# Kernel optimization log

Hardware: AMD Instinct MI355X
Metric: run time of the kernel (lower is better)

## Reference

```python
import jax, jax.numpy as jnp
import numpy as np

EDGE_DIM = 3
NUM_HEADS = 8
HIDDEN = NUM_HEADS * 2  # 16
N = 2048
E = 65536


def setup_inputs() -> dict:
    key = jax.random.key(0)
    k1, k2, k3, k4, k5 = jax.random.split(key, 5)
    # xavier_uniform bounds: sqrt(6/(fan_in+fan_out))
    lim1 = float(np.sqrt(6.0 / (EDGE_DIM + HIDDEN)))
    lim2 = float(np.sqrt(6.0 / (HIDDEN + NUM_HEADS)))
    return {
        "edge_index": jax.random.randint(k1, (2, E), 0, N, dtype=jnp.int64)
        if jax.config.jax_enable_x64 else jax.random.randint(k1, (2, E), 0, N, dtype=jnp.int32),
        "edge_attr": jax.random.normal(k2, (E, EDGE_DIM), dtype=jnp.float32),
        "num_nodes": N,
        "W1": jax.random.uniform(k3, (EDGE_DIM, HIDDEN), jnp.float32, -lim1, lim1),
        "b1": jnp.zeros((HIDDEN,), jnp.float32),
        "W2": jax.random.uniform(k4, (HIDDEN, NUM_HEADS), jnp.float32, -lim2, lim2),
        "b2": jnp.zeros((NUM_HEADS,), jnp.float32),
    }


def reference(edge_index, edge_attr, num_nodes, W1, b1, W2, b2):
    # tiny MLP: (E,3) -> (E,16) -> relu -> (E,8)
    h = jax.nn.relu(edge_attr @ W1 + b1)
    edge_bias = h @ W2 + b2  # (E, H)
    src, dst = edge_index[0], edge_index[1]
    bias = jnp.zeros((num_nodes, num_nodes, NUM_HEADS), dtype=edge_bias.dtype)
    bias = bias.at[src, dst].set(edge_bias)
    return bias
```

## Files before the change

### kernel.cpp

```cpp
#include <hip/hip_runtime.h>
#include <math.h>

#define EDGE_DIM 3
#define NUM_HEADS 8
#define HIDDEN 16

typedef float float4v __attribute__((ext_vector_type(4)));

__device__ __forceinline__ void edge_mlp(const float a0, const float a1, const float a2,
                                         const float* __restrict__ W1,
                                         const float* __restrict__ b1,
                                         const float* __restrict__ W2,
                                         const float* __restrict__ b2,
                                         float* o ) {
    float h[HIDDEN];
#pragma unroll
    for (int j = 0; j < HIDDEN; ++j) {
        float s = b1[j];
        s += a0 * W1[0 * HIDDEN + j];
        s += a1 * W1[1 * HIDDEN + j];
        s += a2 * W1[2 * HIDDEN + j];
        h[j] = s > 0.0f ? s : 0.0f;
    }
#pragma unroll
    for (int i = 0; i < NUM_HEADS; ++i) {
        float s = b2[i];
#pragma unroll
        for (int j = 0; j < HIDDEN; ++j) s += h[j] * W2[j * NUM_HEADS + i];
        o[i] = s;
    }
}

__global__ void k_mark(const int* __restrict__ ei, float* __restrict__ out,
                       int E, int N) {
    int e = blockIdx.x * blockDim.x + threadIdx.x;
    if (e >= E) return;
    int src = ei[e];
    int dst = ei[E + e];
    size_t slot = (size_t)src * (size_t)N + (size_t)dst;
    unsigned* p = (unsigned*)(out + slot * NUM_HEADS);
    atomicMax(p, (unsigned)(e + 1));
}

__global__ void k_write(const int* __restrict__ ei, const float* __restrict__ ea,
                        const float* __restrict__ W1, const float* __restrict__ b1,
                        const float* __restrict__ W2, const float* __restrict__ b2,
                        float* __restrict__ out, int E, int N) {
    int e = blockIdx.x * blockDim.x + threadIdx.x;
    if (e >= E) return;
    int src = ei[e];
    int dst = ei[E + e];
    size_t slot = (size_t)src * (size_t)N + (size_t)dst;
    float* p = out + slot * NUM_HEADS;
    unsigned m = *(const unsigned*)p;
    if (m != (unsigned)(e + 1)) return;
    float o[NUM_HEADS];
    edge_mlp(ea[e * EDGE_DIM + 0], ea[e * EDGE_DIM + 1], ea[e * EDGE_DIM + 2],
             W1, b1, W2, b2, o);
    unsigned u = __float_as_uint(o[0]);
    if (u >= 1u && u <= (unsigned)E) o[0] = 0.0f;
    float4v lo = {o[0], o[1], o[2], o[3]};
    float4v hi = {o[4], o[5], o[6], o[7]};
    *(float4v*)p = lo;
    *(float4v*)(p + 4) = hi;
}

extern "C" void kernel_launch(void* const* d_in, const int* in_sizes, int n_in,
                              void* d_out, int out_size, void* d_ws, size_t ws_size,
                              hipStream_t stream) {
    const int* ei   = (const int*)d_in[0];
    const float* ea = (const float*)d_in[1];
    const float* W1 = (const float*)d_in[3];
    const float* b1 = (const float*)d_in[4];
    const float* W2 = (const float*)d_in[5];
    const float* b2 = (const float*)d_in[6];
    float* out = (float*)d_out;

    const int E = in_sizes[0] / 2;
    const int N = (int)(sqrt((double)(out_size / NUM_HEADS)) + 0.5);

    hipMemsetAsync(d_out, 0, (size_t)out_size * sizeof(float), stream);

    const int blk = 256;
    const int grid = (E + blk - 1) / blk;
    k_mark<<<grid, blk, 0, stream>>>(ei, out, E, N);
    k_write<<<grid, blk, 0, stream>>>(ei, ea, W1, b1, W2, b2, out, E, N);
}
```

Baseline: 33.06 us.

## Use compact workspace marker and fused fill kernel instead of output memset

When workspace is large enough, atomic last-writer markers go into a compact N*N uint array and per-edge MLP results into a workspace buffer. A single fill kernel then writes the whole output once, either zeros or the gathered edge bias, which replaces the full-output memset followed by scattered writes. The memset shrinks eightfold, but the fill kernel still writes the full 134MB output and adds a marker read plus indirect gathers. If the workspace is too small, the old path is kept as a fallback.

```diff
diff --git a/kernel.cpp b/kernel.cpp
--- a/kernel.cpp
+++ b/kernel.cpp
@@ -31,26 +31,58 @@
     }
 }
 
-__global__ void k_mark(const int* __restrict__ ei, float* __restrict__ out,
-                       int E, int N) {
+__global__ void k_mark_mlp(const int* __restrict__ ei, const float* __restrict__ ea,
+                           const float* __restrict__ W1, const float* __restrict__ b1,
+                           const float* __restrict__ W2, const float* __restrict__ b2,
+                           unsigned* __restrict__ marker, float4v* __restrict__ ebias,
+                           int E, int N) {
     int e = blockIdx.x * blockDim.x + threadIdx.x;
     if (e >= E) return;
+    float o[NUM_HEADS];
+    edge_mlp(ea[e * EDGE_DIM + 0], ea[e * EDGE_DIM + 1], ea[e * EDGE_DIM + 2],
+             W1, b1, W2, b2, o);
+    float4v lo = {o[0], o[1], o[2], o[3]};
+    float4v hi = {o[4], o[5], o[6], o[7]};
+    ebias[(size_t)e * 2 + 0] = lo;
+    ebias[(size_t)e * 2 + 1] = hi;
     int src = ei[e];
     int dst = ei[E + e];
     size_t slot = (size_t)src * (size_t)N + (size_t)dst;
-    unsigned* p = (unsigned*)(out + slot * NUM_HEADS);
-    atomicMax(p, (unsigned)(e + 1));
+    atomicMax(&marker[slot], (unsigned)(e + 1));
 }
 
-__global__ void k_write(const int* __restrict__ ei, const float* __restrict__ ea,
-                        const float* __restrict__ W1, const float* __restrict__ b1,
-                        const float* __restrict__ W2, const float* __restrict__ b2,
-                        float* __restrict__ out, int E, int N) {
+__global__ void k_fill(const unsigned* __restrict__ marker,
+                       const float4v* __restrict__ ebias,
+                       float4v* __restrict__ out, size_t nslots) {
+    size_t s = (size_t)blockIdx.x * blockDim.x + threadIdx.x;
+    if (s >= nslots) return;
+    unsigned m = marker[s];
+    float4v lo = {0.0f, 0.0f, 0.0f, 0.0f};
+    float4v hi = {0.0f, 0.0f, 0.0f, 0.0f};
+    if (m) {
+        size_t e = (size_t)(m - 1);
+        lo = ebias[e * 2 + 0];
+        hi = ebias[e * 2 + 1];
+    }
+    out[s * 2 + 0] = lo;
+    out[s * 2 + 1] = hi;
+}
+
+__global__ void k_mark_out(const int* __restrict__ ei, float* __restrict__ out,
+                           int E, int N) {
     int e = blockIdx.x * blockDim.x + threadIdx.x;
     if (e >= E) return;
-    int src = ei[e];
-    int dst = ei[E + e];
-    size_t slot = (size_t)src * (size_t)N + (size_t)dst;
+    size_t slot = (size_t)ei[e] * (size_t)N + (size_t)ei[E + e];
+    atomicMax((unsigned*)(out + slot * NUM_HEADS), (unsigned)(e + 1));
+}
+
+__global__ void k_write_out(const int* __restrict__ ei, const float* __restrict__ ea,
+                            const float* __restrict__ W1, const float* __restrict__ b1,
+                            const float* __restrict__ W2, const float* __restrict__ b2,
+                            float* __restrict__ out, int E, int N) {
+    int e = blockIdx.x * blockDim.x + threadIdx.x;
+    if (e >= E) return;
+    size_t slot = (size_t)ei[e] * (size_t)N + (size_t)ei[E + e];
     float* p = out + slot * NUM_HEADS;
     unsigned m = *(const unsigned*)p;
     if (m != (unsigned)(e + 1)) return;
@@ -78,11 +110,25 @@
 
     const int E = in_sizes[0] / 2;
     const int N = (int)(sqrt((double)(out_size / NUM_HEADS)) + 0.5);
+    const size_t nslots = (size_t)N * (size_t)N;
 
-    hipMemsetAsync(d_out, 0, (size_t)out_size * sizeof(float), stream);
+    const size_t marker_bytes = nslots * sizeof(unsigned);
+    const size_t ebias_bytes  = (size_t)E * NUM_HEADS * sizeof(float);
+    const int blk = 256;
+    const int egrid = (E + blk - 1) / blk;
 
-    const int blk = 256;
-    const int grid = (E + blk - 1) / blk;
-    k_mark<<<grid, blk, 0, stream>>>(ei, out, E, N);
-    k_write<<<grid, blk, 0, stream>>>(ei, ea, W1, b1, W2, b2, out, E, N);
+    if (ws_size >= marker_bytes + ebias_bytes) {
+        unsigned* marker = (unsigned*)d_ws;
+        float4v* ebias = (float4v*)((char*)d_ws + marker_bytes);
+
+        hipMemsetAsync(marker, 0, marker_bytes, stream);
+        k_mark_mlp<<<egrid, blk, 0, stream>>>(ei, ea, W1, b1, W2, b2,
+                                              marker, ebias, E, N);
+        const size_t sgrid = (nslots + blk - 1) / blk;
+        k_fill<<<(int)sgrid, blk, 0, stream>>>(marker, ebias, (float4v*)out, nslots);
+    } else {
+        hipMemsetAsync(d_out, 0, (size_t)out_size * sizeof(float), stream);
+        k_mark_out<<<egrid, blk, 0, stream>>>(ei, out, E, N);
+        k_write_out<<<egrid, blk, 0, stream>>>(ei, ea, W1, b1, W2, b2, out, E, N);
+    }
 }
```

After: 43.63 us. 1.32x slower.

## Replace output memset with bitmap-guided fill kernel that writes every slot

Applied to the files above, without the earlier changes.

Drops the full-output memset. The mark pass now resolves last-writer tags with a CAS loop and records touched slots in a workspace bitmap. A new fill kernel then writes every 16-byte output unit, emitting either zeros or the MLP result of the winning edge. The aim is to merge the clear and the scatter into one streaming write pass. The cost is extra bitmap traffic and reliance on workspace and output contents that are never cleared between calls: bmA only accumulates bits, and bmB is only ever cleared. This risks wrong results if stale tags or stale bits from earlier runs collide with the current edges.

```diff
diff --git a/kernel.cpp b/kernel.cpp
--- a/kernel.cpp
+++ b/kernel.cpp
@@ -32,25 +32,73 @@
 }
 
 __global__ void k_mark(const int* __restrict__ ei, float* __restrict__ out,
+                       unsigned long long* __restrict__ bmA,
+                       unsigned long long* __restrict__ bmB,
                        int E, int N) {
     int e = blockIdx.x * blockDim.x + threadIdx.x;
     if (e >= E) return;
-    int src = ei[e];
-    int dst = ei[E + e];
-    size_t slot = (size_t)src * (size_t)N + (size_t)dst;
+    size_t slot = (size_t)ei[e] * (size_t)N + (size_t)ei[E + e];
     unsigned* p = (unsigned*)(out + slot * NUM_HEADS);
-    atomicMax(p, (unsigned)(e + 1));
+    const unsigned my = (unsigned)(e + 1);
+
+    unsigned w = atomicOr(p, 0u);
+    while (true) {
+        bool is_tag = (w >= 1u && w <= (unsigned)E);
+        if (is_tag && w >= my) break;
+        unsigned old = atomicCAS(p, w, my);
+        if (old == w) break;
+        w = old;
+    }
+    atomicOr(&bmA[slot >> 6], 1ull << (slot & 63));
+    atomicAnd(&bmB[slot >> 6], ~(1ull << (slot & 63)));
 }
 
-__global__ void k_write(const int* __restrict__ ei, const float* __restrict__ ea,
-                        const float* __restrict__ W1, const float* __restrict__ b1,
-                        const float* __restrict__ W2, const float* __restrict__ b2,
-                        float* __restrict__ out, int E, int N) {
+__global__ __launch_bounds__(256) void k_fill(
+        const unsigned long long* __restrict__ bmA,
+        const unsigned long long* __restrict__ bmB,
+        const int* __restrict__ ei, const float* __restrict__ ea,
+        const float* __restrict__ W1, const float* __restrict__ b1,
+        const float* __restrict__ W2, const float* __restrict__ b2,
+        float4v* __restrict__ out4, int E, int N, size_t nunits) {
+    size_t u = (size_t)blockIdx.x * 256 + threadIdx.x;
+    if (u >= nunits) return;
+    size_t s = u >> 1;
+    float4v v = {0.0f, 0.0f, 0.0f, 0.0f};
+    unsigned long long bm = bmA[s >> 6] & ~bmB[s >> 6];
+    if ((bm >> (s & 63)) & 1ull) {
+        unsigned t = ((const unsigned*)&out4[s << 1])[0];
+        if (t >= 1u && t <= (unsigned)E) {
+            unsigned e = t - 1u;
+            size_t es = (size_t)ei[e] * (size_t)N + (size_t)ei[(size_t)E + e];
+            if (es == s) {
+                float o[NUM_HEADS];
+                edge_mlp(ea[(size_t)e * EDGE_DIM + 0], ea[(size_t)e * EDGE_DIM + 1],
+                         ea[(size_t)e * EDGE_DIM + 2], W1, b1, W2, b2, o);
+                unsigned u0 = __float_as_uint(o[0]);
+                if (u0 >= 1u && u0 <= (unsigned)E) o[0] = 0.0f;
+                if (u & 1) { v[0] = o[4]; v[1] = o[5]; v[2] = o[6]; v[3] = o[7]; }
+                else       { v[0] = o[0]; v[1] = o[1]; v[2] = o[2]; v[3] = o[3]; }
+            }
+        }
+    }
+    out4[u] = v;
+}
+
+__global__ void k_mark_out(const int* __restrict__ ei, float* __restrict__ out,
+                           int E, int N) {
     int e = blockIdx.x * blockDim.x + threadIdx.x;
     if (e >= E) return;
-    int src = ei[e];
-    int dst = ei[E + e];
-    size_t slot = (size_t)src * (size_t)N + (size_t)dst;
+    size_t slot = (size_t)ei[e] * (size_t)N + (size_t)ei[E + e];
+    atomicMax((unsigned*)(out + slot * NUM_HEADS), (unsigned)(e + 1));
+}
+
+__global__ void k_write_out(const int* __restrict__ ei, const float* __restrict__ ea,
+                            const float* __restrict__ W1, const float* __restrict__ b1,
+                            const float* __restrict__ W2, const float* __restrict__ b2,
+                            float* __restrict__ out, int E, int N) {
+    int e = blockIdx.x * blockDim.x + threadIdx.x;
+    if (e >= E) return;
+    size_t slot = (size_t)ei[e] * (size_t)N + (size_t)ei[E + e];
     float* p = out + slot * NUM_HEADS;
     unsigned m = *(const unsigned*)p;
     if (m != (unsigned)(e + 1)) return;
@@ -78,11 +126,23 @@
 
     const int E = in_sizes[0] / 2;
     const int N = (int)(sqrt((double)(out_size / NUM_HEADS)) + 0.5);
-
-    hipMemsetAsync(d_out, 0, (size_t)out_size * sizeof(float), stream);
+    const size_t nslots = (size_t)N * (size_t)N;
+    const size_t nunits = nslots * 2;
+    const size_t nwords = (nslots + 63) / 64;
 
     const int blk = 256;
-    const int grid = (E + blk - 1) / blk;
-    k_mark<<<grid, blk, 0, stream>>>(ei, out, E, N);
-    k_write<<<grid, blk, 0, stream>>>(ei, ea, W1, b1, W2, b2, out, E, N);
+    const int egrid = (E + blk - 1) / blk;
+
+    if (ws_size >= 2 * nwords * sizeof(unsigned long long)) {
+        unsigned long long* bmA = (unsigned long long*)d_ws;
+        unsigned long long* bmB = bmA + nwords;
+        k_mark<<<egrid, blk, 0, stream>>>(ei, out, bmA, bmB, E, N);
+        const int fgrid = (int)((nunits + blk - 1) / blk);
+        k_fill<<<fgrid, blk, 0, stream>>>(bmA, bmB, ei, ea, W1, b1, W2, b2,
+                                          (float4v*)out, E, N, nunits);
+    } else {
+        hipMemsetAsync(d_out, 0, (size_t)out_size * sizeof(float), stream);
+        k_mark_out<<<egrid, blk, 0, stream>>>(ei, out, E, N);
+        k_write_out<<<egrid, blk, 0, stream>>>(ei, ea, W1, b1, W2, b2, out, E, N);
+    }
 }
```

Result: slower. 56.83 us (+71.9%).
